# Kernel tuning notes

Hardware: AMD Instinct MI355X
Metric: run time of the kernel (lower is better)

Reference implementation:

```python
import jax, jax.numpy as jnp
import numpy as np

B, TV, TH, F, H, D = 16, 128, 64, 512, 512, 256


def setup_inputs() -> dict:
    key = jax.random.key(0)
    ks = jax.random.split(key, 6)
    return {
        "v": jax.random.normal(ks[0], (B, TV, F), dtype=jnp.float32),
        "h": jax.random.normal(ks[1], (B, TH, H), dtype=jnp.float32),
        "W": jax.random.normal(ks[2], (F, D), dtype=jnp.float32) * 0.05,
        "U": jax.random.normal(ks[3], (H, D), dtype=jnp.float32) * 0.05,
        "b": jax.random.normal(ks[4], (D,), dtype=jnp.float32) * 0.05,
        "w": jax.random.normal(ks[5], (D, 1), dtype=jnp.float32) * 0.05,
    }


def reference(v, h, W, U, b, w):
    # v: [B, Tv, F] video features; h: [B, Th, H] decoder hidden states
    Wv = jnp.einsum("btf,fd->btd", v, W)      # [B, Tv, D]
    Uh = jnp.einsum("bsh,hd->bsd", h, U)      # [B, Th, D]
    # Broadcast add -> [B, Th, Tv, D], tanh nonlinearity (additive attention)
    f = jnp.tanh(Uh[:, :, None, :] + Wv[:, None, :, :] + b)
    q = jnp.einsum("bstd,d->bst", f, w[:, 0])  # scores [B, Th, Tv]
    beta = jax.nn.softmax(q, axis=-1)           # softmax over Tv (axis -2 of q[..., None])
    u = jnp.einsum("bst,btf->bsf", beta, v)    # context [B, Th, F]
    return u
```

## Files before the change

kernel.cpp:

```cpp
#include <hip/hip_runtime.h>
#include <hip/hip_bf16.h>

#define BB 16
#define TV 128
#define TH 64
#define FF 512
#define HH 512
#define DD 256

#define LOG2E2 2.8853900817779268f

typedef __attribute__((ext_vector_type(8))) short bf16x8;
typedef __attribute__((ext_vector_type(4))) float f32x4;

__device__ __forceinline__ float fast_exp2(float x) {
#if __has_builtin(__builtin_amdgcn_exp2f)
  return __builtin_amdgcn_exp2f(x);
#else
  return __expf(x * 0.6931471805599453f);
#endif
}
__device__ __forceinline__ float fast_rcp(float x) {
#if __has_builtin(__builtin_amdgcn_rcpf)
  return __builtin_amdgcn_rcpf(x);
#else
  return 1.0f / x;
#endif
}
__device__ __forceinline__ unsigned short f2bf(float x) {
  union { float f; unsigned u; } a; a.f = x;
  unsigned r = a.u + 0x7fffu + ((a.u >> 16) & 1u);
  return (unsigned short)(r >> 16);
}

#define NT_V 262144
#define NT_H 131072
#define NT_W 32768
__global__ __launch_bounds__(256) void convert_kernel(
    const float* __restrict__ v, const float* __restrict__ h,
    const float* __restrict__ W, const float* __restrict__ U,
    unsigned short* __restrict__ vb, unsigned short* __restrict__ hb,
    unsigned short* __restrict__ WT, unsigned short* __restrict__ UT) {
  int task = blockIdx.x * 256 + threadIdx.x;
  if (task < NT_V) {
    float4 x = ((const float4*)v)[task];
    ushort4 o = make_ushort4(f2bf(x.x), f2bf(x.y), f2bf(x.z), f2bf(x.w));
    *(ushort4*)&vb[(size_t)task * 4] = o;
  } else if (task < NT_V + NT_H) {
    int t2 = task - NT_V;
    float4 x = ((const float4*)h)[t2];
    ushort4 o = make_ushort4(f2bf(x.x), f2bf(x.y), f2bf(x.z), f2bf(x.w));
    *(ushort4*)&hb[(size_t)t2 * 4] = o;
  } else {
    int t2 = task - NT_V - NT_H;
    const float* S;
    unsigned short* Dt;
    if (t2 < NT_W) { S = W; Dt = WT; } else { S = U; Dt = UT; t2 -= NT_W; }
    int n = t2 & 255, k4 = t2 >> 8;
    float a0 = S[(k4 * 4 + 0) * 256 + n];
    float a1 = S[(k4 * 4 + 1) * 256 + n];
    float a2 = S[(k4 * 4 + 2) * 256 + n];
    float a3 = S[(k4 * 4 + 3) * 256 + n];
    ushort4 o = make_ushort4(f2bf(a0), f2bf(a1), f2bf(a2), f2bf(a3));
    *(ushort4*)&Dt[(size_t)n * 512 + k4 * 4] = o;
  }
}

__global__ __launch_bounds__(128) void mfma_gemm_kernel(
    const unsigned short* __restrict__ Av, const unsigned short* __restrict__ Ah,
    const unsigned short* __restrict__ WT, const unsigned short* __restrict__ UT,
    const float* __restrict__ bias, float* __restrict__ Wv2,
    float* __restrict__ Uh2) {
  const int bid = blockIdx.x;
  const unsigned short* A;
  const unsigned short* BT;
  const float* bi;
  float* C;
  int mt, nt;
  if (bid < 256) {
    A = Av; BT = WT; C = Wv2; bi = nullptr;
    mt = bid >> 3; nt = bid & 7;
  } else {
    const int b2 = bid - 256;
    A = Ah; BT = UT; C = Uh2; bi = bias;
    mt = b2 >> 3; nt = b2 & 7;
  }
  const int wv   = threadIdx.x >> 6;
  const int lane = threadIdx.x & 63;
  const int m0   = mt * 64 + wv * 32;
  const int n0   = nt * 32;
  const int r16  = lane & 15;
  const int quad = lane >> 4;

  const unsigned short* a0p = A + (size_t)(m0 + r16) * 512 + quad * 8;
  const unsigned short* a1p = a0p + 16 * 512;
  const unsigned short* b0p = BT + (size_t)(n0 + r16) * 512 + quad * 8;
  const unsigned short* b1p = b0p + 16 * 512;

  f32x4 acc00 = {0.f, 0.f, 0.f, 0.f};
  f32x4 acc01 = {0.f, 0.f, 0.f, 0.f};
  f32x4 acc10 = {0.f, 0.f, 0.f, 0.f};
  f32x4 acc11 = {0.f, 0.f, 0.f, 0.f};

#pragma unroll
  for (int kc = 0; kc < 16; kc++) {
    bf16x8 a0 = *(const bf16x8*)(a0p + kc * 32);
    bf16x8 a1 = *(const bf16x8*)(a1p + kc * 32);
    bf16x8 b0 = *(const bf16x8*)(b0p + kc * 32);
    bf16x8 b1 = *(const bf16x8*)(b1p + kc * 32);
    acc00 = __builtin_amdgcn_mfma_f32_16x16x32_bf16(a0, b0, acc00, 0, 0, 0);
    acc01 = __builtin_amdgcn_mfma_f32_16x16x32_bf16(a0, b1, acc01, 0, 0, 0);
    acc10 = __builtin_amdgcn_mfma_f32_16x16x32_bf16(a1, b0, acc10, 0, 0, 0);
    acc11 = __builtin_amdgcn_mfma_f32_16x16x32_bf16(a1, b1, acc11, 0, 0, 0);
  }

  const float bj0 = bi ? bi[n0 + r16] : 0.0f;
  const float bj1 = bi ? bi[n0 + 16 + r16] : 0.0f;
#pragma unroll
  for (int r = 0; r < 4; r++) {
    const int row0 = m0 + quad * 4 + r;
    C[(size_t)row0 * 256 + n0 + r16]            = (acc00[r] + bj0) * LOG2E2;
    C[(size_t)row0 * 256 + n0 + 16 + r16]       = (acc01[r] + bj1) * LOG2E2;
    C[(size_t)(row0 + 16) * 256 + n0 + r16]     = (acc10[r] + bj0) * LOG2E2;
    C[(size_t)(row0 + 16) * 256 + n0 + 16 + r16] = (acc11[r] + bj1) * LOG2E2;
  }
}

__global__ __launch_bounds__(1024) void attn_fused_kernel(
    const float* __restrict__ Wv2, const float* __restrict__ Uh2,
    const float* __restrict__ wg, const float* __restrict__ v,
    float* __restrict__ u) {
  __shared__ float UhS[4 * 256];
  __shared__ float wS[256];
  __shared__ float pS[1024];
  __shared__ float bS[4 * 128];
  __shared__ float mW[8];
  __shared__ float sW[8];

  const int tid = threadIdx.x;
  const int b   = blockIdx.x >> 4;
  const int sg  = blockIdx.x & 15;
  const int s0  = sg * 4;

  if (tid < 256) {
    const int row = tid >> 6, q4 = (tid & 63) << 2;
    *(float4*)&UhS[row * 256 + q4] =
        *(const float4*)&Uh2[(size_t)(b * 64 + s0 + row) * 256 + q4];
  } else if (tid < 320) {
    const int q4 = (tid - 256) << 2;
    *(float4*)&wS[q4] = *(const float4*)&wg[q4];
  }
  __syncthreads();

  {
    const int t    = tid & 127;
    const int dh   = (tid >> 7) & 1;
    const int s_sc = tid >> 8;
    const float4* wvrow = (const float4*)(Wv2 + (size_t)(b * 128 + t) * 256) + dh * 32;
    const float4* uhrow = (const float4*)&UhS[s_sc * 256] + dh * 32;
    const float4* wrow  = (const float4*)&wS[0] + dh * 32;
    float acc = 0.0f;
#pragma unroll 8
    for (int j = 0; j < 32; j++) {
      float4 a  = wvrow[j];
      float4 uh = uhrow[j];
      float4 ww = wrow[j];
      acc = fmaf(ww.x, fast_rcp(fast_exp2(a.x + uh.x) + 1.0f), acc);
      acc = fmaf(ww.y, fast_rcp(fast_exp2(a.y + uh.y) + 1.0f), acc);
      acc = fmaf(ww.z, fast_rcp(fast_exp2(a.z + uh.z) + 1.0f), acc);
      acc = fmaf(ww.w, fast_rcp(fast_exp2(a.w + uh.w) + 1.0f), acc);
    }
    pS[tid] = acc;
  }
  __syncthreads();

  float qv = 0.0f, ev = 0.0f;
  const int wvid = tid >> 6, lane = tid & 63;
  if (tid < 512) {
    const int s_l = tid >> 7, t = tid & 127;
    qv = (pS[s_l * 256 + t] + pS[s_l * 256 + 128 + t]) * (-LOG2E2);
    float m = qv;
#pragma unroll
    for (int off = 32; off > 0; off >>= 1) m = fmaxf(m, __shfl_xor(m, off, 64));
    if (lane == 0) mW[wvid] = m;
  }
  __syncthreads();
  if (tid < 512) {
    float m = fmaxf(mW[wvid], mW[wvid ^ 1]);
    ev = fast_exp2(qv - m);
    float ssum = ev;
#pragma unroll
    for (int off = 32; off > 0; off >>= 1) ssum += __shfl_xor(ssum, off, 64);
    if (lane == 0) sW[wvid] = ssum;
  }
  __syncthreads();
  if (tid < 512) {
    const int s_l = tid >> 7, t = tid & 127;
    bS[s_l * 128 + t] = ev * fast_rcp(sW[wvid] + sW[wvid ^ 1]);
  }
  __syncthreads();

  const float* vb2 = v + (size_t)b * TV * FF;
  const int f  = tid & 511;
  const int sh = tid >> 9;
  float a0 = 0.f, a1 = 0.f;
#pragma unroll 4
  for (int tg = 0; tg < 128; tg += 4) {
    float4 b0 = *(const float4*)&bS[(sh * 2 + 0) * 128 + tg];
    float4 b1 = *(const float4*)&bS[(sh * 2 + 1) * 128 + tg];
    float v0 = vb2[(tg + 0) * 512 + f];
    float v1 = vb2[(tg + 1) * 512 + f];
    float v2 = vb2[(tg + 2) * 512 + f];
    float v3 = vb2[(tg + 3) * 512 + f];
    a0 = fmaf(b0.x, v0, a0); a0 = fmaf(b0.y, v1, a0);
    a0 = fmaf(b0.z, v2, a0); a0 = fmaf(b0.w, v3, a0);
    a1 = fmaf(b1.x, v0, a1); a1 = fmaf(b1.y, v1, a1);
    a1 = fmaf(b1.z, v2, a1); a1 = fmaf(b1.w, v3, a1);
  }
  float* urow = u + (size_t)(b * 64 + s0 + sh * 2) * 512;
  urow[0 * 512 + f] = a0;
  urow[1 * 512 + f] = a1;
}

extern "C" void kernel_launch(void* const* d_in, const int* in_sizes, int n_in,
                              void* d_out, int out_size, void* d_ws, size_t ws_size,
                              hipStream_t stream) {
  const float* v  = (const float*)d_in[0];
  const float* h  = (const float*)d_in[1];
  const float* W  = (const float*)d_in[2];
  const float* U  = (const float*)d_in[3];
  const float* bb = (const float*)d_in[4];
  const float* w  = (const float*)d_in[5];
  float* u = (float*)d_out;

  float* Wv2 = (float*)d_ws;
  float* Uh2 = Wv2 + (size_t)2048 * 256;
  unsigned short* vb16 = (unsigned short*)(Uh2 + (size_t)1024 * 256);
  unsigned short* hb16 = vb16 + (size_t)2048 * 512;
  unsigned short* WT   = hb16 + (size_t)1024 * 512;
  unsigned short* UT   = WT + (size_t)256 * 512;

  convert_kernel<<<1792, 256, 0, stream>>>(v, h, W, U, vb16, hb16, WT, UT);
  mfma_gemm_kernel<<<384, 128, 0, stream>>>(vb16, hb16, WT, UT, bb, Wv2, Uh2);
  attn_fused_kernel<<<256, 1024, 0, stream>>>(Wv2, Uh2, w, v, u);
}
```

Before: 100.7 us.

## Store Wv transposed per batch and remap score-phase threads for coalesced loads

The GEMM epilogue now writes Wv in a per-batch [D][Tv] transposed layout. The score phase is remapped so each thread handles four consecutive t values over a 32-wide slice of D, giving coalesced float4 global loads and broadcast LDS reads of Uh and w. Partial sums now span eight D-groups, which enlarges the shared partial buffer to 16 KB and adds an eight-way reduction before the softmax. The transposed epilogue stores are strided and less coalesced, so the GEMM's write cost may rise.

```diff
diff --git a/kernel.cpp b/kernel.cpp
--- a/kernel.cpp
+++ b/kernel.cpp
@@ -69,20 +69,19 @@
 __global__ __launch_bounds__(128) void mfma_gemm_kernel(
     const unsigned short* __restrict__ Av, const unsigned short* __restrict__ Ah,
     const unsigned short* __restrict__ WT, const unsigned short* __restrict__ UT,
-    const float* __restrict__ bias, float* __restrict__ Wv2,
+    const float* __restrict__ bias, float* __restrict__ Wv2T,
     float* __restrict__ Uh2) {
   const int bid = blockIdx.x;
   const unsigned short* A;
   const unsigned short* BT;
-  const float* bi;
-  float* C;
   int mt, nt;
+  bool is_wv;
   if (bid < 256) {
-    A = Av; BT = WT; C = Wv2; bi = nullptr;
+    A = Av; BT = WT; is_wv = true;
     mt = bid >> 3; nt = bid & 7;
   } else {
     const int b2 = bid - 256;
-    A = Ah; BT = UT; C = Uh2; bi = bias;
+    A = Ah; BT = UT; is_wv = false;
     mt = b2 >> 3; nt = b2 & 7;
   }
   const int wv   = threadIdx.x >> 6;
@@ -114,25 +113,38 @@
     acc11 = __builtin_amdgcn_mfma_f32_16x16x32_bf16(a1, b1, acc11, 0, 0, 0);
   }
 
-  const float bj0 = bi ? bi[n0 + r16] : 0.0f;
-  const float bj1 = bi ? bi[n0 + 16 + r16] : 0.0f;
-#pragma unroll
-  for (int r = 0; r < 4; r++) {
-    const int row0 = m0 + quad * 4 + r;
-    C[(size_t)row0 * 256 + n0 + r16]            = (acc00[r] + bj0) * LOG2E2;
-    C[(size_t)row0 * 256 + n0 + 16 + r16]       = (acc01[r] + bj1) * LOG2E2;
-    C[(size_t)(row0 + 16) * 256 + n0 + r16]     = (acc10[r] + bj0) * LOG2E2;
-    C[(size_t)(row0 + 16) * 256 + n0 + 16 + r16] = (acc11[r] + bj1) * LOG2E2;
+  if (is_wv) {
+    const int bb   = m0 >> 7;
+    const int tb   = (m0 & 127) + quad * 4;
+    float* Wb = Wv2T + (size_t)bb * 32768;
+#pragma unroll
+    for (int r = 0; r < 4; r++) {
+      Wb[(size_t)(n0 + r16) * 128 + tb + r]        = acc00[r] * LOG2E2;
+      Wb[(size_t)(n0 + 16 + r16) * 128 + tb + r]   = acc01[r] * LOG2E2;
+      Wb[(size_t)(n0 + r16) * 128 + tb + 16 + r]   = acc10[r] * LOG2E2;
+      Wb[(size_t)(n0 + 16 + r16) * 128 + tb + 16 + r] = acc11[r] * LOG2E2;
+    }
+  } else {
+    const float bj0 = bias[n0 + r16];
+    const float bj1 = bias[n0 + 16 + r16];
+#pragma unroll
+    for (int r = 0; r < 4; r++) {
+      const int row0 = m0 + quad * 4 + r;
+      Uh2[(size_t)row0 * 256 + n0 + r16]             = (acc00[r] + bj0) * LOG2E2;
+      Uh2[(size_t)row0 * 256 + n0 + 16 + r16]        = (acc01[r] + bj1) * LOG2E2;
+      Uh2[(size_t)(row0 + 16) * 256 + n0 + r16]      = (acc10[r] + bj0) * LOG2E2;
+      Uh2[(size_t)(row0 + 16) * 256 + n0 + 16 + r16] = (acc11[r] + bj1) * LOG2E2;
+    }
   }
 }
 
 __global__ __launch_bounds__(1024) void attn_fused_kernel(
-    const float* __restrict__ Wv2, const float* __restrict__ Uh2,
+    const float* __restrict__ Wv2T, const float* __restrict__ Uh2,
     const float* __restrict__ wg, const float* __restrict__ v,
     float* __restrict__ u) {
   __shared__ float UhS[4 * 256];
   __shared__ float wS[256];
-  __shared__ float pS[1024];
+  __shared__ float pS[4 * 1024];
   __shared__ float bS[4 * 128];
   __shared__ float mW[8];
   __shared__ float sW[8];
@@ -153,24 +165,24 @@
   __syncthreads();
 
   {
-    const int t    = tid & 127;
-    const int dh   = (tid >> 7) & 1;
-    const int s_sc = tid >> 8;
-    const float4* wvrow = (const float4*)(Wv2 + (size_t)(b * 128 + t) * 256) + dh * 32;
-    const float4* uhrow = (const float4*)&UhS[s_sc * 256] + dh * 32;
-    const float4* wrow  = (const float4*)&wS[0] + dh * 32;
-    float acc = 0.0f;
+    const int t4 = tid & 31;
+    const int dg = (tid >> 5) & 7;
+    const int s  = tid >> 8;
+    const float* wvb = Wv2T + (size_t)b * 32768 + (size_t)dg * 32 * 128 + t4 * 4;
+    const float* uhp = &UhS[s * 256 + dg * 32];
+    const float* wp  = &wS[dg * 32];
+    float4 acc = {0.f, 0.f, 0.f, 0.f};
 #pragma unroll 8
     for (int j = 0; j < 32; j++) {
-      float4 a  = wvrow[j];
-      float4 uh = uhrow[j];
-      float4 ww = wrow[j];
-      acc = fmaf(ww.x, fast_rcp(fast_exp2(a.x + uh.x) + 1.0f), acc);
-      acc = fmaf(ww.y, fast_rcp(fast_exp2(a.y + uh.y) + 1.0f), acc);
-      acc = fmaf(ww.z, fast_rcp(fast_exp2(a.z + uh.z) + 1.0f), acc);
-      acc = fmaf(ww.w, fast_rcp(fast_exp2(a.w + uh.w) + 1.0f), acc);
+      float4 a  = *(const float4*)(wvb + j * 128);
+      float uh = uhp[j];
+      float ww = wp[j];
+      acc.x = fmaf(ww, fast_rcp(fast_exp2(a.x + uh) + 1.0f), acc.x);
+      acc.y = fmaf(ww, fast_rcp(fast_exp2(a.y + uh) + 1.0f), acc.y);
+      acc.z = fmaf(ww, fast_rcp(fast_exp2(a.z + uh) + 1.0f), acc.z);
+      acc.w = fmaf(ww, fast_rcp(fast_exp2(a.w + uh) + 1.0f), acc.w);
     }
-    pS[tid] = acc;
+    *(float4*)&pS[s * 1024 + dg * 128 + t4 * 4] = acc;
   }
   __syncthreads();
 
@@ -178,7 +190,10 @@
   const int wvid = tid >> 6, lane = tid & 63;
   if (tid < 512) {
     const int s_l = tid >> 7, t = tid & 127;
-    qv = (pS[s_l * 256 + t] + pS[s_l * 256 + 128 + t]) * (-LOG2E2);
+    float ssum = 0.0f;
+#pragma unroll
+    for (int dg = 0; dg < 8; dg++) ssum += pS[s_l * 1024 + dg * 128 + t];
+    qv = ssum * (-LOG2E2);
     float m = qv;
 #pragma unroll
     for (int off = 32; off > 0; off >>= 1) m = fmaxf(m, __shfl_xor(m, off, 64));
@@ -233,14 +248,14 @@
   const float* w  = (const float*)d_in[5];
   float* u = (float*)d_out;
 
-  float* Wv2 = (float*)d_ws;
-  float* Uh2 = Wv2 + (size_t)2048 * 256;
+  float* Wv2T = (float*)d_ws;
+  float* Uh2  = Wv2T + (size_t)2048 * 256;
   unsigned short* vb16 = (unsigned short*)(Uh2 + (size_t)1024 * 256);
   unsigned short* hb16 = vb16 + (size_t)2048 * 512;
   unsigned short* WT   = hb16 + (size_t)1024 * 512;
   unsigned short* UT   = WT + (size_t)256 * 512;
 
   convert_kernel<<<1792, 256, 0, stream>>>(v, h, W, U, vb16, hb16, WT, UT);
-  mfma_gemm_kernel<<<384, 128, 0, stream>>>(vb16, hb16, WT, UT, bb, Wv2, Uh2);
-  attn_fused_kernel<<<256, 1024, 0, stream>>>(Wv2, Uh2, w, v, u);
-}
+  mfma_gemm_kernel<<<384, 128, 0, stream>>>(vb16, hb16, WT, UT, bb, Wv2T, Uh2);
+  attn_fused_kernel<<<256, 1024, 0, stream>>>(Wv2T, Uh2, w, v, u);
+}
```

Result: faster. 92.87 us (-7.8%).
